# Optimization experiments

Measured on AMD Instinct MI355X. Metric: run time of the kernel, lower is better.

## Reference

```python
import jax, jax.numpy as jnp
import numpy as np

# init config (from module __init__ / docstring example)
VOXEL_SIZE = np.array([0.2, 0.2, 8.0], dtype=np.float32)
PC_RANGE = np.array([0.0, -25.6, -3.0, 51.2, 25.6, 5.0], dtype=np.float32)
MAX_PTS = 32
MAX_VOX = 16000
GRID = (int((PC_RANGE[3] - PC_RANGE[0]) / VOXEL_SIZE[0]),
        int((PC_RANGE[4] - PC_RANGE[1]) / VOXEL_SIZE[1]),
        int((PC_RANGE[5] - PC_RANGE[2]) / VOXEL_SIZE[2]))  # (256, 256, 1)

N_POINTS = 4_000_000
C_FEAT = 4  # xyz + intensity


def setup_inputs() -> dict:
    key = jax.random.key(0)
    u = jax.random.uniform(key, (N_POINTS, C_FEAT), dtype=jnp.float32)
    lo = jnp.array([PC_RANGE[0], PC_RANGE[1], PC_RANGE[2], 0.0], jnp.float32)
    span = jnp.array([PC_RANGE[3] - PC_RANGE[0], PC_RANGE[4] - PC_RANGE[1],
                      PC_RANGE[5] - PC_RANGE[2], 1.0], jnp.float32)
    points = u * span + lo  # uniformly inside the point-cloud range
    return {"points": points}


def reference(points):
    """Hard voxelization. Returns fixed-size (padded) outputs:
    voxels [MAX_VOX, MAX_PTS, C], coords [MAX_VOX, 3] int32, num_points [MAX_VOX] int32.
    Unused voxel slots are zero (num_points==0), matching torch semantics up to padding."""
    N, C = points.shape
    Gx, Gy, Gz = GRID
    lo = jnp.asarray(PC_RANGE[:3])
    hi = jnp.asarray(PC_RANGE[3:])
    vsz = jnp.asarray(VOXEL_SIZE)

    xyz = points[:, :3]
    valid = jnp.all((xyz >= lo) & (xyz < hi), axis=1)  # in-range mask

    coords = jnp.floor((xyz - lo) / vsz).astype(jnp.int32)
    coords = jnp.clip(coords, 0, jnp.array([Gx - 1, Gy - 1, Gz - 1], jnp.int32))

    # linear voxel hash; invalid points get sentinel so they sort to the end
    BIG = Gx * Gy * Gz
    vhash = coords[:, 0] * (Gy * Gz) + coords[:, 1] * Gz + coords[:, 2]
    vhash = jnp.where(valid, vhash, BIG)

    order = jnp.argsort(vhash)
    sh = vhash[order]          # [N] sorted hashes
    sc = coords[order]         # [N,3]
    sp = points[order]         # [N,C]
    svalid = sh < BIG

    # segment boundaries of the sorted hash stream (== torch.unique inverse groups)
    newv = jnp.concatenate([jnp.array([True]), sh[1:] != sh[:-1]]) & svalid
    vid = jnp.cumsum(newv.astype(jnp.int32)) - 1   # voxel id per point (sorted order)

    idx = jnp.arange(N, dtype=jnp.int32)
    start = jax.lax.cummax(jnp.where(newv, idx, 0))  # index of first point of own voxel
    rank = idx - start                                # position within voxel

    keep = svalid & (rank < MAX_PTS) & (vid < MAX_VOX)
    vid_s = jnp.where(keep, vid, MAX_VOX)   # route dropped points to dump row
    rank_s = jnp.where(keep, rank, 0)

    voxels = jnp.zeros((MAX_VOX + 1, MAX_PTS, C), points.dtype)
    voxels = voxels.at[vid_s, rank_s].set(sp)[:MAX_VOX]

    cvid = jnp.where(newv & (vid < MAX_VOX), vid, MAX_VOX)
    coords_out = jnp.zeros((MAX_VOX + 1, 3), jnp.int32).at[cvid].set(sc)[:MAX_VOX]

    num_points = jax.ops.segment_sum(keep.astype(jnp.int32), vid_s,
                                     num_segments=MAX_VOX + 1)[:MAX_VOX]
    return voxels, coords_out, num_points
```

## Files before the change

### kernel.cpp

```cpp
#include <hip/hip_runtime.h>

#define NBINS    65536
#define NWORDS   16384
#define MAXVOX   16000
#define MAXPTS   32
#define NBLK     256
#define RSEG     8

#define COORDS_OFF (MAXVOX * MAXPTS * 4)
#define NP_OFF     (COORDS_OFF + MAXVOX * 3)

#define OFF_COUNTS   0u
#define OFF_STARTS   (256u << 10)
#define OFF_BINOF    (512u << 10)
#define OFF_PARTC    (576u << 10)
#define OFF_PARTO    (577u << 10)
#define OFF_BASEC    (578u << 10)
#define OFF_BASEO    (579u << 10)
#define OFF_BINS     (1u << 20)
#define OFF_PARTIAL  (17u << 20)
#define OFF_MEMBERS  (33u << 20)

__global__ __launch_bounds__(1024) void k_hist(const float4* __restrict__ pts, int n,
                                               unsigned* __restrict__ bins,
                                               unsigned* __restrict__ partial) {
    __shared__ unsigned sh[NWORDS];
    int t = threadIdx.x, b = blockIdx.x;
    for (int w = t; w < NWORDS; w += 1024) sh[w] = 0u;
    __syncthreads();

    int chunk = (n + NBLK - 1) / NBLK;
    int s = b * chunk;
    int e = min(n, s + chunk);
    for (int i = s + t; i < e; i += 1024) {
        float4 p = pts[i];
        bool valid = (p.x >= 0.0f)   & (p.x < 51.2f) &
                     (p.y >= -25.6f) & (p.y < 25.6f) &
                     (p.z >= -3.0f)  & (p.z < 5.0f);
        int cx = (int)floorf((p.x - 0.0f)  / 0.2f);
        int cy = (int)floorf((p.y + 25.6f) / 0.2f);
        int cz = (int)floorf((p.z + 3.0f)  / 8.0f);
        cx = min(max(cx, 0), 255);
        cy = min(max(cy, 0), 255);
        cz = min(max(cz, 0), 0);
        unsigned bin = (unsigned)(cx * 256 + cy + cz);
        if (valid) {
            bins[i] = bin;
            atomicAdd(&sh[bin >> 2], 1u << ((bin & 3u) * 8u));
        } else {
            bins[i] = 0xFFFFFFFFu;
        }
    }
    __syncthreads();
    unsigned* myp = partial + (size_t)b * NWORDS;
    for (int w = t; w < NWORDS; w += 1024) myp[w] = sh[w];
}

__global__ __launch_bounds__(512) void k_reduce(unsigned* __restrict__ partial,
                                                unsigned* __restrict__ counts,
                                                unsigned* __restrict__ partC,
                                                unsigned* __restrict__ partO) {
    __shared__ unsigned segsum[RSEG][64][4];
    __shared__ unsigned red[512];
    int t = threadIdx.x;
    int wl  = t & 63;
    int seg = t >> 6;
    int w   = blockIdx.x * 64 + wl;
    int blk0 = seg * (NBLK / RSEG);

    unsigned a0 = 0, a1 = 0, a2 = 0, a3 = 0;
    for (int b = 0; b < NBLK / RSEG; ++b) {
        unsigned v = partial[(size_t)(blk0 + b) * NWORDS + w];
        a0 += v & 255u; a1 += (v >> 8) & 255u;
        a2 += (v >> 16) & 255u; a3 += (v >> 24) & 255u;
    }
    segsum[seg][wl][0] = a0; segsum[seg][wl][1] = a1;
    segsum[seg][wl][2] = a2; segsum[seg][wl][3] = a3;
    __syncthreads();

    unsigned b0 = 0, b1 = 0, b2 = 0, b3 = 0;
    for (int s2 = 0; s2 < seg; ++s2) {
        b0 += segsum[s2][wl][0]; b1 += segsum[s2][wl][1];
        b2 += segsum[s2][wl][2]; b3 += segsum[s2][wl][3];
    }
    for (int b = 0; b < NBLK / RSEG; ++b) {
        size_t idx = (size_t)(blk0 + b) * NWORDS + w;
        unsigned v = partial[idx];
        partial[idx] = b0 | (b1 << 8) | (b2 << 16) | (b3 << 24);
        b0 += v & 255u; b1 += (v >> 8) & 255u;
        b2 += (v >> 16) & 255u; b3 += (v >> 24) & 255u;
    }

    unsigned mySum = 0, myOcc = 0;
    if (seg == RSEG - 1) {
        counts[w * 4 + 0] = b0; counts[w * 4 + 1] = b1;
        counts[w * 4 + 2] = b2; counts[w * 4 + 3] = b3;
        mySum = b0 + b1 + b2 + b3;
        myOcc = (b0 > 0u) + (b1 > 0u) + (b2 > 0u) + (b3 > 0u);
    }
    red[t] = mySum; __syncthreads();
    for (int off = 256; off > 0; off >>= 1) { if (t < off) red[t] += red[t + off]; __syncthreads(); }
    if (t == 0) partC[blockIdx.x] = red[0];
    __syncthreads();
    red[t] = myOcc; __syncthreads();
    for (int off = 256; off > 0; off >>= 1) { if (t < off) red[t] += red[t + off]; __syncthreads(); }
    if (t == 0) partO[blockIdx.x] = red[0];
}

__global__ void k_scan2(const unsigned* __restrict__ partC, const unsigned* __restrict__ partO,
                        unsigned* __restrict__ baseC, unsigned* __restrict__ baseO) {
    __shared__ unsigned sc[256], so[256];
    int t = threadIdx.x;
    unsigned mc = partC[t], mo = partO[t];
    sc[t] = mc; so[t] = mo;
    __syncthreads();
    for (int off = 1; off < 256; off <<= 1) {
        unsigned ac = (t >= off) ? sc[t - off] : 0u;
        unsigned ao = (t >= off) ? so[t - off] : 0u;
        __syncthreads();
        sc[t] += ac; so[t] += ao;
        __syncthreads();
    }
    baseC[t] = sc[t] - mc;
    baseO[t] = so[t] - mo;
}

__global__ void k_scan3(const unsigned* __restrict__ counts,
                        const unsigned* __restrict__ baseC, const unsigned* __restrict__ baseO,
                        unsigned* __restrict__ starts, unsigned* __restrict__ binof,
                        float* __restrict__ out) {
    __shared__ unsigned sc[256], so[256];
    int t = threadIdx.x;
    int bin = blockIdx.x * 256 + t;
    unsigned c = counts[bin];
    unsigned occ = (c > 0u) ? 1u : 0u;
    sc[t] = c; so[t] = occ;
    __syncthreads();
    for (int off = 1; off < 256; off <<= 1) {
        unsigned ac = (t >= off) ? sc[t - off] : 0u;
        unsigned ao = (t >= off) ? so[t - off] : 0u;
        __syncthreads();
        sc[t] += ac; so[t] += ao;
        __syncthreads();
    }
    unsigned st  = baseC[blockIdx.x] + (sc[t] - c);
    unsigned vid = baseO[blockIdx.x] + (so[t] - occ);
    bool kept = occ && (vid < MAXVOX);
    starts[bin] = st | (kept ? 0u : 0x80000000u);
    if (kept) {
        binof[vid] = (unsigned)bin;
        out[COORDS_OFF + vid * 3 + 0] = (float)(bin >> 8);
        out[COORDS_OFF + vid * 3 + 1] = (float)(bin & 255);
        out[COORDS_OFF + vid * 3 + 2] = 0.0f;
        out[NP_OFF + vid] = (float)(c < MAXPTS ? c : MAXPTS);
    }
}

__global__ __launch_bounds__(1024) void k_scatter(const unsigned* __restrict__ bins, int n,
                                                  const unsigned* __restrict__ partial,
                                                  const unsigned* __restrict__ starts,
                                                  unsigned* __restrict__ members) {
    __shared__ unsigned sh[NWORDS];
    int t = threadIdx.x, b = blockIdx.x;
    const unsigned* myp = partial + (size_t)b * NWORDS;
    for (int w = t; w < NWORDS; w += 1024) sh[w] = myp[w];
    __syncthreads();

    int chunk = (n + NBLK - 1) / NBLK;
    int s = b * chunk;
    int e = min(n, s + chunk);
    for (int i = s + t; i < e; i += 1024) {
        unsigned v = bins[i];
        if (v == 0xFFFFFFFFu) continue;
        unsigned st = starts[v];
        if (st & 0x80000000u) continue;
        unsigned old = atomicAdd(&sh[v >> 2], 1u << ((v & 3u) * 8u));
        unsigned off = (old >> ((v & 3u) * 8u)) & 255u;
        members[st + off] = (unsigned)i;
    }
}

__global__ __launch_bounds__(256) void k_select(
        const unsigned* __restrict__ binof, const unsigned* __restrict__ counts,
        const unsigned* __restrict__ starts, const unsigned* __restrict__ members,
        const float4* __restrict__ pts, float4* __restrict__ vox) {
    int v = blockIdx.x * 4 + (threadIdx.x >> 6);
    unsigned lane = threadIdx.x & 63u;
    unsigned bin = binof[v];
    if (bin == 0xFFFFFFFFu) return;
    unsigned m  = counts[bin];
    unsigned mc = m > 256u ? 256u : m;
    unsigned start = starts[bin] & 0x7FFFFFFFu;

    if (mc <= 64u) {
        unsigned e0 = (lane < mc) ? members[start + lane] : 0xFFFFFFFFu;
        unsigned r0 = 0;
        int jm = (int)mc;
        for (int j = 0; j < jm; ++j) {
            unsigned a0 = (unsigned)__shfl((int)e0, j);
            r0 += (a0 < e0);
        }
        if (e0 != 0xFFFFFFFFu && r0 < MAXPTS) vox[(size_t)v * MAXPTS + r0] = pts[e0];
    } else if (mc <= 128u) {
        unsigned e0 = members[start + lane];
        unsigned e1 = (lane + 64u < mc) ? members[start + lane + 64u] : 0xFFFFFFFFu;
        unsigned r0 = 0, r1 = 0;
        for (int j = 0; j < 64; ++j) {
            unsigned a0 = (unsigned)__shfl((int)e0, j);
            unsigned a1 = (unsigned)__shfl((int)e1, j);
            r0 += (a0 < e0) + (a1 < e0);
            r1 += (a0 < e1) + (a1 < e1);
        }
        if (r0 < MAXPTS) vox[(size_t)v * MAXPTS + r0] = pts[e0];
        if (e1 != 0xFFFFFFFFu && r1 < MAXPTS) vox[(size_t)v * MAXPTS + r1] = pts[e1];
    } else {
        unsigned e0 = members[start + lane];
        unsigned e1 = members[start + lane + 64u];
        unsigned e2 = (lane + 128u < mc) ? members[start + lane + 128u] : 0xFFFFFFFFu;
        unsigned e3 = (lane + 192u < mc) ? members[start + lane + 192u] : 0xFFFFFFFFu;
        unsigned r0 = 0, r1 = 0, r2 = 0, r3 = 0;
        for (int j = 0; j < 64; ++j) {
            unsigned a0 = (unsigned)__shfl((int)e0, j);
            unsigned a1 = (unsigned)__shfl((int)e1, j);
            unsigned a2 = (unsigned)__shfl((int)e2, j);
            unsigned a3 = (unsigned)__shfl((int)e3, j);
            r0 += (a0 < e0) + (a1 < e0) + (a2 < e0) + (a3 < e0);
            r1 += (a0 < e1) + (a1 < e1) + (a2 < e1) + (a3 < e1);
            r2 += (a0 < e2) + (a1 < e2) + (a2 < e2) + (a3 < e2);
            r3 += (a0 < e3) + (a1 < e3) + (a2 < e3) + (a3 < e3);
        }
        if (r0 < MAXPTS) vox[(size_t)v * MAXPTS + r0] = pts[e0];
        if (r1 < MAXPTS) vox[(size_t)v * MAXPTS + r1] = pts[e1];
        if (e2 != 0xFFFFFFFFu && r2 < MAXPTS) vox[(size_t)v * MAXPTS + r2] = pts[e2];
        if (e3 != 0xFFFFFFFFu && r3 < MAXPTS) vox[(size_t)v * MAXPTS + r3] = pts[e3];
    }
}

extern "C" void kernel_launch(void* const* d_in, const int* in_sizes, int n_in,
                              void* d_out, int out_size, void* d_ws, size_t ws_size,
                              hipStream_t stream) {
    const float4* pts = (const float4*)d_in[0];
    int n = in_sizes[0] / 4;
    float* out = (float*)d_out;
    char* ws = (char*)d_ws;

    unsigned* counts  = (unsigned*)(ws + OFF_COUNTS);
    unsigned* starts  = (unsigned*)(ws + OFF_STARTS);
    unsigned* binof   = (unsigned*)(ws + OFF_BINOF);
    unsigned* partC   = (unsigned*)(ws + OFF_PARTC);
    unsigned* partO   = (unsigned*)(ws + OFF_PARTO);
    unsigned* baseC   = (unsigned*)(ws + OFF_BASEC);
    unsigned* baseO   = (unsigned*)(ws + OFF_BASEO);
    unsigned* bins    = (unsigned*)(ws + OFF_BINS);
    unsigned* partial = (unsigned*)(ws + OFF_PARTIAL);
    unsigned* members = (unsigned*)(ws + OFF_MEMBERS);

    hipMemsetAsync(d_out, 0, (size_t)out_size * sizeof(float), stream);
    hipMemsetAsync(binof, 0xFF, MAXVOX * sizeof(unsigned), stream);

    k_hist   <<<NBLK, 1024, 0, stream>>>(pts, n, bins, partial);
    k_reduce <<<NWORDS / 64, 512, 0, stream>>>(partial, counts, partC, partO);
    k_scan2  <<<1, 256, 0, stream>>>(partC, partO, baseC, baseO);
    k_scan3  <<<256, 256, 0, stream>>>(counts, baseC, baseO, starts, binof, out);
    k_scatter<<<NBLK, 1024, 0, stream>>>(bins, n, partial, starts, members);
    k_select <<<MAXVOX / 4, 256, 0, stream>>>(binof, counts, starts, members, pts, (float4*)d_out);
}
```

Baseline: 87.29 us.

## Drop memsets and scan2 kernel by folding init and prefix into neighbors

Removes the two hipMemsetAsync calls. The binof sentinel init moves into k_reduce, and k_select now writes zeros for empty voxel rows, coords and counts, so the whole output is no longer zeroed. The single-block k_scan2 is merged into k_scan3: each block reduces the partial sums of the blocks before it. This cuts two launches, one serial tiny kernel and about 8 MB of redundant output zeroing, at the cost of a small extra reduction in every scan block.

```diff
diff --git a/kernel.cpp b/kernel.cpp
--- a/kernel.cpp
+++ b/kernel.cpp
@@ -15,8 +15,6 @@
 #define OFF_BINOF    (512u << 10)
 #define OFF_PARTC    (576u << 10)
 #define OFF_PARTO    (577u << 10)
-#define OFF_BASEC    (578u << 10)
-#define OFF_BASEO    (579u << 10)
 #define OFF_BINS     (1u << 20)
 #define OFF_PARTIAL  (17u << 20)
 #define OFF_MEMBERS  (33u << 20)
@@ -59,10 +57,14 @@
 __global__ __launch_bounds__(512) void k_reduce(unsigned* __restrict__ partial,
                                                 unsigned* __restrict__ counts,
                                                 unsigned* __restrict__ partC,
-                                                unsigned* __restrict__ partO) {
+                                                unsigned* __restrict__ partO,
+                                                unsigned* __restrict__ binof) {
     __shared__ unsigned segsum[RSEG][64][4];
     __shared__ unsigned red[512];
     int t = threadIdx.x;
+    int g = blockIdx.x * 512 + t;
+    if (g < MAXVOX) binof[g] = 0xFFFFFFFFu;
+
     int wl  = t & 63;
     int seg = t >> 6;
     int w   = blockIdx.x * 64 + wl;
@@ -107,13 +109,27 @@
     if (t == 0) partO[blockIdx.x] = red[0];
 }
 
-__global__ void k_scan2(const unsigned* __restrict__ partC, const unsigned* __restrict__ partO,
-                        unsigned* __restrict__ baseC, unsigned* __restrict__ baseO) {
-    __shared__ unsigned sc[256], so[256];
+__global__ __launch_bounds__(256) void k_scan3(const unsigned* __restrict__ counts,
+                                               const unsigned* __restrict__ partC,
+                                               const unsigned* __restrict__ partO,
+                                               unsigned* __restrict__ starts,
+                                               unsigned* __restrict__ binof,
+                                               float* __restrict__ out) {
+    __shared__ unsigned rc[256], ro[256], sc[256], so[256];
     int t = threadIdx.x;
-    unsigned mc = partC[t], mo = partO[t];
-    sc[t] = mc; so[t] = mo;
-    __syncthreads();
+    int bin = blockIdx.x * 256 + t;
+    unsigned c = counts[bin];
+    unsigned occ = (c > 0u) ? 1u : 0u;
+
+    rc[t] = (t < blockIdx.x) ? partC[t] : 0u;
+    ro[t] = (t < blockIdx.x) ? partO[t] : 0u;
+    sc[t] = c; so[t] = occ;
+    __syncthreads();
+    for (int off = 128; off > 0; off >>= 1) {
+        if (t < off) { rc[t] += rc[t + off]; ro[t] += ro[t + off]; }
+        __syncthreads();
+    }
+    unsigned baseC = rc[0], baseO = ro[0];
     for (int off = 1; off < 256; off <<= 1) {
         unsigned ac = (t >= off) ? sc[t - off] : 0u;
         unsigned ao = (t >= off) ? so[t - off] : 0u;
@@ -121,30 +137,8 @@
         sc[t] += ac; so[t] += ao;
         __syncthreads();
     }
-    baseC[t] = sc[t] - mc;
-    baseO[t] = so[t] - mo;
-}
-
-__global__ void k_scan3(const unsigned* __restrict__ counts,
-                        const unsigned* __restrict__ baseC, const unsigned* __restrict__ baseO,
-                        unsigned* __restrict__ starts, unsigned* __restrict__ binof,
-                        float* __restrict__ out) {
-    __shared__ unsigned sc[256], so[256];
-    int t = threadIdx.x;
-    int bin = blockIdx.x * 256 + t;
-    unsigned c = counts[bin];
-    unsigned occ = (c > 0u) ? 1u : 0u;
-    sc[t] = c; so[t] = occ;
-    __syncthreads();
-    for (int off = 1; off < 256; off <<= 1) {
-        unsigned ac = (t >= off) ? sc[t - off] : 0u;
-        unsigned ao = (t >= off) ? so[t - off] : 0u;
-        __syncthreads();
-        sc[t] += ac; so[t] += ao;
-        __syncthreads();
-    }
-    unsigned st  = baseC[blockIdx.x] + (sc[t] - c);
-    unsigned vid = baseO[blockIdx.x] + (so[t] - occ);
+    unsigned st  = baseC + (sc[t] - c);
+    unsigned vid = baseO + (so[t] - occ);
     bool kept = occ && (vid < MAXVOX);
     starts[bin] = st | (kept ? 0u : 0x80000000u);
     if (kept) {
@@ -183,14 +177,24 @@
 __global__ __launch_bounds__(256) void k_select(
         const unsigned* __restrict__ binof, const unsigned* __restrict__ counts,
         const unsigned* __restrict__ starts, const unsigned* __restrict__ members,
-        const float4* __restrict__ pts, float4* __restrict__ vox) {
+        const float4* __restrict__ pts, float* __restrict__ out) {
+    float4* vox = (float4*)out;
     int v = blockIdx.x * 4 + (threadIdx.x >> 6);
     unsigned lane = threadIdx.x & 63u;
+    const float4 z4 = {0.0f, 0.0f, 0.0f, 0.0f};
     unsigned bin = binof[v];
-    if (bin == 0xFFFFFFFFu) return;
+    if (bin == 0xFFFFFFFFu) {
+        if (lane < 32u) vox[(size_t)v * MAXPTS + lane] = z4;
+        if (lane < 3u)  out[COORDS_OFF + v * 3 + lane] = 0.0f;
+        if (lane == 3u) out[NP_OFF + v] = 0.0f;
+        return;
+    }
     unsigned m  = counts[bin];
     unsigned mc = m > 256u ? 256u : m;
+    unsigned np = m > 32u ? 32u : m;
     unsigned start = starts[bin] & 0x7FFFFFFFu;
+
+    if (lane >= np && lane < 32u) vox[(size_t)v * MAXPTS + lane] = z4;
 
     if (mc <= 64u) {
         unsigned e0 = (lane < mc) ? members[start + lane] : 0xFFFFFFFFu;
@@ -249,19 +253,13 @@
     unsigned* binof   = (unsigned*)(ws + OFF_BINOF);
     unsigned* partC   = (unsigned*)(ws + OFF_PARTC);
     unsigned* partO   = (unsigned*)(ws + OFF_PARTO);
-    unsigned* baseC   = (unsigned*)(ws + OFF_BASEC);
-    unsigned* baseO   = (unsigned*)(ws + OFF_BASEO);
     unsigned* bins    = (unsigned*)(ws + OFF_BINS);
     unsigned* partial = (unsigned*)(ws + OFF_PARTIAL);
     unsigned* members = (unsigned*)(ws + OFF_MEMBERS);
 
-    hipMemsetAsync(d_out, 0, (size_t)out_size * sizeof(float), stream);
-    hipMemsetAsync(binof, 0xFF, MAXVOX * sizeof(unsigned), stream);
-
     k_hist   <<<NBLK, 1024, 0, stream>>>(pts, n, bins, partial);
-    k_reduce <<<NWORDS / 64, 512, 0, stream>>>(partial, counts, partC, partO);
-    k_scan2  <<<1, 256, 0, stream>>>(partC, partO, baseC, baseO);
-    k_scan3  <<<256, 256, 0, stream>>>(counts, baseC, baseO, starts, binof, out);
+    k_reduce <<<NWORDS / 64, 512, 0, stream>>>(partial, counts, partC, partO, binof);
+    k_scan3  <<<256, 256, 0, stream>>>(counts, partC, partO, starts, binof, out);
     k_scatter<<<NBLK, 1024, 0, stream>>>(bins, n, partial, starts, members);
-    k_select <<<MAXVOX / 4, 256, 0, stream>>>(binof, counts, starts, members, pts, (float4*)d_out);
-}
+    k_select <<<MAXVOX / 4, 256, 0, stream>>>(binof, counts, starts, members, pts, out);
+}
```

Measured after the change: 76.81 us. 1.14x faster.
